# Optimization experiments

Measured on AMD Instinct MI355X. Metric: run time of the kernel, lower is better.

Reference implementation:

```python
import jax, jax.numpy as jnp
import numpy as np

N, E = 100000, 3200000
F_NODE, F_EDGE = 2, 7
H, C = 4, 8
HC = H * C
REG, TGT = 500, 1
NUM_LAYERS = 3
ATT_SLOPE = 0.2   # LeakyReLU inside GATv2 attention
ACT_SLOPE = 0.01  # model-level LeakyReLU default
BN_EPS = 1e-5


def gatv2(x, src, dst, e_attr, Wl, bl, Wr, br, We, att, bias):
    n = x.shape[0]
    xl = (x @ Wl + bl).reshape(n, H, C)          # source transform (messages)
    xr = (x @ Wr + br).reshape(n, H, C)          # destination transform
    ee = (e_attr @ We).reshape(-1, H, C)         # edge transform (no bias in PyG)
    m = jax.nn.leaky_relu(xl[src] + xr[dst] + ee, ATT_SLOPE)  # [Ef,H,C]
    logits = jnp.einsum('ehc,hc->eh', m, att)    # [Ef,H]
    mx = jax.ops.segment_max(logits, dst, num_segments=n)
    ex = jnp.exp(logits - mx[dst])
    den = jax.ops.segment_sum(ex, dst, num_segments=n)
    alpha = ex / (den[dst] + 1e-16)              # edge-softmax grouped by dst
    out = jax.ops.segment_sum(xl[src] * alpha[:, :, None], dst, num_segments=n)
    return out.reshape(n, HC) + bias             # concat heads + bias


def setup_inputs() -> dict:
    key = jax.random.key(0)
    ks = jax.random.split(key, 30)
    # edges with no self loops (module calls add_self_loops on top)
    s = jax.random.randint(ks[0], (E,), 0, N, dtype=jnp.int32)
    off = jax.random.randint(ks[1], (E,), 1, N, dtype=jnp.int32)
    d = (s + off) % N
    edge_index = jnp.stack([s, d])
    x = jax.random.normal(ks[2], (N, F_NODE), dtype=jnp.float32)
    edge_attr = jax.random.normal(ks[3], (E, F_EDGE), dtype=jnp.float32)

    def glorot(k, shape):
        fan = shape[0] + shape[-1]
        return jax.random.normal(k, shape, dtype=jnp.float32) * jnp.sqrt(2.0 / fan)

    inp = dict(x=x, edge_index=edge_index, edge_attr=edge_attr)
    i = 4
    for tag, fin in (("1", F_NODE), ("2", HC)):
        inp["Wl" + tag] = glorot(ks[i], (fin, HC)); i += 1
        inp["bl" + tag] = jnp.zeros((HC,), jnp.float32)
        inp["Wr" + tag] = glorot(ks[i], (fin, HC)); i += 1
        inp["br" + tag] = jnp.zeros((HC,), jnp.float32)
        inp["We" + tag] = glorot(ks[i], (F_EDGE, HC)); i += 1
        inp["att" + tag] = glorot(ks[i], (H, C)); i += 1
        inp["b" + tag] = jnp.zeros((HC,), jnp.float32)
    inp["gamma"] = jnp.ones((HC,), jnp.float32)
    inp["beta"] = jnp.zeros((HC,), jnp.float32)
    inp["Wreg"] = glorot(ks[i], (HC, REG)); i += 1
    inp["breg"] = jnp.zeros((REG,), jnp.float32)
    inp["Wend"] = glorot(ks[i], (REG, TGT)); i += 1
    inp["bend"] = jnp.zeros((TGT,), jnp.float32)
    return inp


def reference(x, edge_index, edge_attr,
              Wl1, bl1, Wr1, br1, We1, att1, b1,
              Wl2, bl2, Wr2, br2, We2, att2, b2,
              gamma, beta, Wreg, breg, Wend, bend):
    n = x.shape[0]
    loop = jnp.arange(n, dtype=edge_index.dtype)
    srcf = jnp.concatenate([edge_index[0], loop])
    dstf = jnp.concatenate([edge_index[1], loop])
    # self-loop edge attrs filled with mean (PyG fill_value='mean')
    ea_mean = jnp.mean(edge_attr, axis=0, keepdims=True)
    eaf = jnp.concatenate([edge_attr, jnp.broadcast_to(ea_mean, (n, edge_attr.shape[1]))])

    h = gatv2(x, srcf, dstf, eaf, Wl1, bl1, Wr1, br1, We1, att1, b1)
    for _ in range(NUM_LAYERS - 1):
        mu = jnp.mean(h, axis=0)
        var = jnp.var(h, axis=0)
        h = (h - mu) * jax.lax.rsqrt(var + BN_EPS) * gamma + beta
        h = jax.nn.leaky_relu(h, ACT_SLOPE)
        h = gatv2(h, srcf, dstf, eaf, Wl2, bl2, Wr2, br2, We2, att2, b2)
    h = jax.nn.leaky_relu(h, ACT_SLOPE)
    h = h @ Wreg + breg
    return h @ Wend + bend
```

## Files before the change

### kernel.cpp

```cpp
#include <hip/hip_runtime.h>
#include <hip/hip_fp16.h>
#include <math.h>

#define NN 100000
#define EE 3200000
#define FE 7
#define GNB 32
#define CRR 1024
#define NBK 391
#define BKCAP 8688
#define T1 4096
#define FB1 ((EE + T1 - 1) / T1)

typedef unsigned int uivec4 __attribute__((ext_vector_type(4)));
static __device__ __forceinline__ uint4 ntload4(const uint4* p) {
    uivec4 v = __builtin_nontemporal_load((const uivec4*)p);
    uint4 r; r.x = v.x; r.y = v.y; r.z = v.z; r.w = v.w; return r;
}

static __device__ __forceinline__ __half2 hmax2(__half2 a, __half2 b) {
    unsigned int ua = *(unsigned int*)&a, ub = *(unsigned int*)&b, ur;
    asm("v_pk_max_f16 %0, %1, %2" : "=v"(ur) : "v"(ua), "v"(ub));
    return *(__half2*)&ur;
}


__global__ void k_ea_sum(const float* __restrict__ ea, double* __restrict__ ea_sum) {
    float acc[FE];
#pragma unroll
    for (int f = 0; f < FE; ++f) acc[f] = 0.f;
    int stride = gridDim.x * blockDim.x;
    for (int e = blockIdx.x * blockDim.x + threadIdx.x; e < EE; e += stride) {
        const float* r = ea + (size_t)e * FE;
#pragma unroll
        for (int f = 0; f < FE; ++f) acc[f] += r[f];
    }
    __shared__ float part[4][FE];
    int wave = threadIdx.x >> 6;
#pragma unroll
    for (int f = 0; f < FE; ++f) {
        float v = acc[f];
        for (int o = 32; o > 0; o >>= 1) v += __shfl_down(v, o, 64);
        if ((threadIdx.x & 63) == 0) part[wave][f] = v;
    }
    __syncthreads();
    if (threadIdx.x < FE) {
        float s = part[0][threadIdx.x] + part[1][threadIdx.x] +
                  part[2][threadIdx.x] + part[3][threadIdx.x];
        atomicAdd(&ea_sum[threadIdx.x], (double)s);
    }
}

__global__ void k_ea_mean(const double* __restrict__ ea_sum, float* __restrict__ ea_mean) {
    int f = threadIdx.x;
    if (f < 8) ea_mean[f] = (f < FE) ? (float)(ea_sum[f] / (double)EE) : 0.f;
}

__global__ void k_ginit(int* __restrict__ gbucket) {
    int b = blockIdx.x * blockDim.x + threadIdx.x;
    if (b < NBK) gbucket[b] = b * BKCAP;
}

__global__ __launch_bounds__(512) void k_fill1(const int* __restrict__ ei,
                                               const float* __restrict__ ea,
                                               int* __restrict__ gbucket,
                                               uint4* __restrict__ srt) {
    __shared__ int hbin[NBK];
    for (int i = threadIdx.x; i < NBK; i += 512) hbin[i] = 0;
    __syncthreads();
    int e0 = blockIdx.x * T1;
    int rb[8];
#pragma unroll
    for (int i = 0; i < 8; ++i) {
        int e = e0 + i * 512 + threadIdx.x;
        int v = -1;
        if (e < EE) {
            int d = __builtin_nontemporal_load(ei + EE + e);
            int b = d >> 8;
            int r = atomicAdd(&hbin[b], 1);
            v = (r << 17) | ((d & 255) << 9) | b;
        }
        rb[i] = v;
    }
    __syncthreads();
    for (int i = threadIdx.x; i < NBK; i += 512) {
        int c = hbin[i];
        hbin[i] = (c > 0) ? atomicAdd(&gbucket[i], c) : 0;
    }
    __syncthreads();
#pragma unroll
    for (int i = 0; i < 8; ++i) {
        int v = rb[i];
        if (v < 0) continue;
        int e = e0 + i * 512 + threadIdx.x;
        int b = v & 511;
        unsigned dl = (unsigned)((v >> 9) & 255);
        int r = v >> 17;
        int pos = hbin[b] + r;
        int s = __builtin_nontemporal_load(ei + e);
        const float* rr = ea + (size_t)e * FE;
        unsigned h[FE];
#pragma unroll
        for (int f = 0; f < FE; ++f) {
            float af = __builtin_nontemporal_load(rr + f);
            h[f] = (unsigned)__half_as_ushort(__float2half_rn(af));
        }
#pragma unroll
        for (int f = 0; f < 6; ++f) { h[f] = (h[f] + 1) >> 1; if (h[f] > 0x7FFFu) h[f] = 0x7FFFu; }
        unsigned h6 = (h[6] + 4) >> 3; if (h6 > 0x1FFFu) h6 = 0x1FFFu;
        uint4 u;
        u.x = h[0] | (h[1] << 15) | ((dl & 3u) << 30);
        u.y = h[2] | (h[3] << 15) | (((dl >> 2) & 3u) << 30);
        u.z = h[4] | (h[5] << 15) | (((dl >> 4) & 3u) << 30);
        u.w = (unsigned)s | (h6 << 17) | ((dl >> 6) << 30);
        srt[(size_t)pos] = u;
    }
}

__global__ __launch_bounds__(512) void k_bscan(const int* __restrict__ gbucket,
                                               int* __restrict__ bbase) {
    __shared__ int ts[512];
    int t = threadIdx.x;
    int c = (t < NBK) ? (gbucket[t] - t * BKCAP) : 0;
    ts[t] = c;
    __syncthreads();
    for (int o = 1; o < 512; o <<= 1) {
        int u = (t >= o) ? ts[t - o] : 0;
        __syncthreads();
        ts[t] += u;
        __syncthreads();
    }
    if (t < NBK) bbase[t] = ts[t] - c;
}

__global__ __launch_bounds__(512) void k_fill2(const uint4* __restrict__ srt,
                                               const int* __restrict__ gbucket,
                                               const int* __restrict__ bbase,
                                               int* __restrict__ offs,
                                               uint4* __restrict__ rec) {
    __shared__ int hist[256], hcopy[256], strt[256];
    int t = threadIdx.x;
    int b = blockIdx.x;
    int nbase = b << 8;
    int nb = NN - nbase; if (nb > 256) nb = 256;
    int sbase = b * BKCAP;
    int cnt = gbucket[b] - sbase;
    int bb = bbase[b];
    if (t < 256) hist[t] = 0;
    __syncthreads();
    for (int p = t; p < cnt; p += 512) {
        uint4 s = srt[(size_t)(sbase + p)];
        int dl = (int)((s.x >> 30) | ((s.y >> 30) << 2) | ((s.z >> 30) << 4) | ((s.w >> 30) << 6));
        atomicAdd(&hist[dl], 1);
    }
    __syncthreads();
    if (t < 256) hcopy[t] = hist[t];
    __syncthreads();
    for (int o = 1; o < 256; o <<= 1) {
        int u = 0;
        if (t < 256 && t >= o) u = hist[t - o];
        __syncthreads();
        if (t < 256) hist[t] += u;
        __syncthreads();
    }
    if (t < 256) {
        int c = hcopy[t];
        int start = bb + hist[t] - c;
        strt[t] = start;
        if (t < nb) offs[nbase + t] = start + c;
    }
    __syncthreads();
    for (int p = t; p < cnt; p += 512) {
        uint4 s = srt[(size_t)(sbase + p)];
        int dl = (int)((s.x >> 30) | ((s.y >> 30) << 2) | ((s.z >> 30) << 4) | ((s.w >> 30) << 6));
        int pos = atomicAdd(&strt[dl], 1);
        uint4 u;
        u.x = ((s.x & 0x7FFFu) << 1) | (((s.x >> 15) & 0x7FFFu) << 17);
        u.y = ((s.y & 0x7FFFu) << 1) | (((s.y >> 15) & 0x7FFFu) << 17);
        u.z = ((s.z & 0x7FFFu) << 1) | (((s.z >> 15) & 0x7FFFu) << 17);
        u.w = (s.w & 0x1FFFFu) | (((s.w >> 17) & 0x1FFFu) << 19);
        rec[(size_t)pos] = u;
    }
}

template <int FIN, bool BN>
__global__ void k_xform(const float* __restrict__ h,
                        const float* __restrict__ Wl, const float* __restrict__ bl,
                        const float* __restrict__ Wr, const float* __restrict__ br,
                        const double* __restrict__ bn_sum, const double* __restrict__ bn_sumsq,
                        const float* __restrict__ gamma, const float* __restrict__ beta,
                        __half* __restrict__ xl, __half* __restrict__ xr) {
    __shared__ float sWl[FIN * 32], sWr[FIN * 32], sb[64];
    __shared__ float smu[FIN], ssc[FIN], sbe[FIN];
    for (int i = threadIdx.x; i < FIN * 32; i += blockDim.x) { sWl[i] = Wl[i]; sWr[i] = Wr[i]; }
    if (threadIdx.x < 32) { sb[threadIdx.x] = bl[threadIdx.x]; sb[32 + threadIdx.x] = br[threadIdx.x]; }
    if (BN && threadIdx.x < FIN) {
        int f = threadIdx.x;
        double mu = bn_sum[f] * (1.0 / NN);
        double var = bn_sumsq[f] * (1.0 / NN) - mu * mu;
        smu[f] = (float)mu;
        ssc[f] = gamma[f] * (float)(1.0 / sqrt(var + 1e-5));
        sbe[f] = beta[f];
    }
    __syncthreads();
    int idx = blockIdx.x * blockDim.x + threadIdx.x;
    if (idx >= NN * 32) return;
    int n = idx >> 5, c = idx & 31;
    const float* hr = h + (size_t)n * FIN;
    float al = sb[c], ar = sb[32 + c];
#pragma unroll
    for (int f = 0; f < FIN; ++f) {
        float v = hr[f];
        if (BN) {
            v = fmaf(v - smu[f], ssc[f], sbe[f]);
            v = v > 0.f ? v : 0.01f * v;
        }
        al = fmaf(v, sWl[f * 32 + c], al);
        ar = fmaf(v, sWr[f * 32 + c], ar);
    }
    xl[idx] = __float2half(al);
    xr[idx] = __float2half(ar);
}

__global__ __launch_bounds__(256) void k_gat_t(
    const int* __restrict__ offs, const uint4* __restrict__ rec,
    const __half* __restrict__ xl, const __half* __restrict__ xr,
    const float* __restrict__ We, const float* __restrict__ att,
    const float* __restrict__ bias, const float* __restrict__ ea_mean,
    float* __restrict__ hout) {
    __shared__ uint4 srec[CRR];
    int n0 = blockIdx.x * GNB;
    int g = threadIdx.x >> 3, j = threadIdx.x & 7, c0 = j * 4;
    int node = n0 + g;

    __half2 weh[FE][2];
#pragma unroll
    for (int f = 0; f < FE; ++f) {
        weh[f][0] = __floats2half2_rn(We[f * 32 + c0], We[f * 32 + c0 + 1]);
        weh[f][1] = __floats2half2_rn(We[f * 32 + c0 + 2], We[f * 32 + c0 + 3]);
    }
    float at0 = att[c0], at1 = att[c0 + 1], at2 = att[c0 + 2], at3 = att[c0 + 3];
    float eam[FE];
#pragma unroll
    for (int f = 0; f < FE; ++f) eam[f] = ea_mean[f];

    float2 rawr = *(const float2*)(xr + (size_t)node * 32 + c0);
    __half2 qh01 = *(const __half2*)&rawr.x;
    __half2 qh23 = *(const __half2*)&rawr.y;
    float2 q01 = __half22float2(qh01);
    float2 q23 = __half22float2(qh23);

    int s_g = (node == 0) ? 0 : offs[node - 1];
    int e_g = offs[node];
    int range0 = (n0 == 0) ? 0 : offs[n0 - 1];
    int range1 = offs[n0 + GNB - 1];

    float sm = 0.f, acc0 = 0.f, acc1 = 0.f, acc2 = 0.f, acc3 = 0.f;
    const __half2 c02 = __float2half2_rn(0.2f);

    auto edge_op = [&](uint4 u, float2 rawl) {
        __half2 lh01 = *(const __half2*)&rawl.x;
        __half2 lh23 = *(const __half2*)&rawl.y;
        __half2 ah01 = *(const __half2*)&u.x;
        __half2 ah23 = *(const __half2*)&u.y;
        __half2 ah45 = *(const __half2*)&u.z;
        __half a6h = __ushort_as_half((unsigned short)((u.w >> 16) & 0xFFFEu));
        __half2 e01 = qh01, e23 = qh23;
        __half2 bc;
        bc = __low2half2(ah01);  e01 = __hfma2(bc, weh[0][0], e01); e23 = __hfma2(bc, weh[0][1], e23);
        bc = __high2half2(ah01); e01 = __hfma2(bc, weh[1][0], e01); e23 = __hfma2(bc, weh[1][1], e23);
        bc = __low2half2(ah23);  e01 = __hfma2(bc, weh[2][0], e01); e23 = __hfma2(bc, weh[2][1], e23);
        bc = __high2half2(ah23); e01 = __hfma2(bc, weh[3][0], e01); e23 = __hfma2(bc, weh[3][1], e23);
        bc = __low2half2(ah45);  e01 = __hfma2(bc, weh[4][0], e01); e23 = __hfma2(bc, weh[4][1], e23);
        bc = __high2half2(ah45); e01 = __hfma2(bc, weh[5][0], e01); e23 = __hfma2(bc, weh[5][1], e23);
        bc = __half2half2(a6h);  e01 = __hfma2(bc, weh[6][0], e01); e23 = __hfma2(bc, weh[6][1], e23);
        __half2 v01 = __hadd2(e01, lh01);
        __half2 v23 = __hadd2(e23, lh23);
        v01 = hmax2(v01, __hmul2(v01, c02));
        v23 = hmax2(v23, __hmul2(v23, c02));
        float2 f01 = __half22float2(v01), f23 = __half22float2(v23);
        float pl = fmaf(f01.x, at0, fmaf(f01.y, at1, fmaf(f23.x, at2, f23.y * at3)));
        float L = pl + __shfl_xor(pl, 1, 64);
        float ex = __expf(L);
        sm += ex;
        float2 l01 = __half22float2(lh01), l23 = __half22float2(lh23);
        acc0 = fmaf(ex, l01.x, acc0);
        acc1 = fmaf(ex, l01.y, acc1);
        acc2 = fmaf(ex, l23.x, acc2);
        acc3 = fmaf(ex, l23.y, acc3);
    };

    for (int base = range0; base < range1; base += CRR) {
        int cnt = range1 - base; if (cnt > CRR) cnt = CRR;
        __syncthreads();
        for (int i = threadIdx.x; i < cnt; i += 256)
            srec[i] = ntload4(&rec[(size_t)base + i]);
        __syncthreads();
        int lo = s_g > base ? s_g : base;
        int hi = e_g < base + cnt ? e_g : base + cnt;
        if (lo >= hi) continue;
        int i1 = lo + 1 < hi ? lo + 1 : hi - 1;
        int i2 = lo + 2 < hi ? lo + 2 : hi - 1;
        uint4 ua = srec[lo - base];
        float2 ra = *(const float2*)(xl + (size_t)(ua.w & 0x1FFFFu) * 32 + c0);
        uint4 ub = srec[i1 - base];
        float2 rb = *(const float2*)(xl + (size_t)(ub.w & 0x1FFFFu) * 32 + c0);
        uint4 uc = srec[i2 - base];
        float2 rc = *(const float2*)(xl + (size_t)(uc.w & 0x1FFFFu) * 32 + c0);
#pragma unroll 3
        for (int p = lo; p < hi; ++p) {
            uint4 cu = ua; float2 cr = ra;
            ua = ub; ra = rb;
            ub = uc; rb = rc;
            int pn = p + 3 < hi ? p + 3 : hi - 1;
            uc = srec[pn - base];
            rc = *(const float2*)(xl + (size_t)(uc.w & 0x1FFFFu) * 32 + c0);
            edge_op(cu, cr);
        }
    }

    {
        float2 rawl = *(const float2*)(xl + (size_t)node * 32 + c0);
        float2 l01 = __half22float2(*(const __half2*)&rawl.x);
        float2 l23 = __half22float2(*(const __half2*)&rawl.y);
        float ee0 = q01.x, ee1 = q01.y, ee2 = q23.x, ee3 = q23.y;
        float wef[FE][4];
#pragma unroll
        for (int f = 0; f < FE; ++f) {
            float2 w0 = __half22float2(weh[f][0]);
            float2 w1 = __half22float2(weh[f][1]);
            wef[f][0] = w0.x; wef[f][1] = w0.y; wef[f][2] = w1.x; wef[f][3] = w1.y;
        }
#pragma unroll
        for (int f = 0; f < FE; ++f) {
            ee0 = fmaf(eam[f], wef[f][0], ee0);
            ee1 = fmaf(eam[f], wef[f][1], ee1);
            ee2 = fmaf(eam[f], wef[f][2], ee2);
            ee3 = fmaf(eam[f], wef[f][3], ee3);
        }
        float v0 = ee0 + l01.x;
        float v1 = ee1 + l01.y;
        float v2 = ee2 + l23.x;
        float v3 = ee3 + l23.y;
        v0 = fmaxf(v0, 0.2f * v0);
        v1 = fmaxf(v1, 0.2f * v1);
        v2 = fmaxf(v2, 0.2f * v2);
        v3 = fmaxf(v3, 0.2f * v3);
        float pl = fmaf(v0, at0, fmaf(v1, at1, fmaf(v2, at2, v3 * at3)));
        float L = pl + __shfl_xor(pl, 1, 64);
        float ex = __expf(L);
        sm += ex;
        acc0 = fmaf(ex, l01.x, acc0);
        acc1 = fmaf(ex, l01.y, acc1);
        acc2 = fmaf(ex, l23.x, acc2);
        acc3 = fmaf(ex, l23.y, acc3);
    }

    float inv = 1.f / (sm + 1e-16f);
    float4 o;
    o.x = fmaf(acc0, inv, bias[c0 + 0]);
    o.y = fmaf(acc1, inv, bias[c0 + 1]);
    o.z = fmaf(acc2, inv, bias[c0 + 2]);
    o.w = fmaf(acc3, inv, bias[c0 + 3]);
    *(float4*)(hout + (size_t)node * 32 + c0) = o;
}

__global__ void k_bn_stats(const float* __restrict__ h, double* __restrict__ bn_sum,
                           double* __restrict__ bn_sumsq) {
    int c = threadIdx.x & 31;
    int row0 = (blockIdx.x * blockDim.x + threadIdx.x) >> 5;
    int rstride = (gridDim.x * blockDim.x) >> 5;
    float s = 0.f, s2 = 0.f;
    for (int n = row0; n < NN; n += rstride) {
        float v = h[(size_t)n * 32 + c];
        s += v;
        s2 = fmaf(v, v, s2);
    }
    s += __shfl_down(s, 32, 64);
    s2 += __shfl_down(s2, 32, 64);
    __shared__ float ls[4][32], ls2[4][32];
    int w = threadIdx.x >> 6;
    if ((threadIdx.x & 63) < 32) { ls[w][c] = s; ls2[w][c] = s2; }
    __syncthreads();
    if (threadIdx.x < 32) {
        float tsum = 0.f, tsq = 0.f;
        for (int i = 0; i < 4; ++i) { tsum += ls[i][threadIdx.x]; tsq += ls2[i][threadIdx.x]; }
        atomicAdd(&bn_sum[threadIdx.x], (double)tsum);
        atomicAdd(&bn_sumsq[threadIdx.x], (double)tsq);
    }
}

__global__ void k_wend(const float* __restrict__ Wreg, const float* __restrict__ breg,
                       const float* __restrict__ Wend, const float* __restrict__ bend,
                       float* __restrict__ wend, float* __restrict__ c0v) {
    int t = threadIdx.x;
    if (t < 32) {
        float s = 0.f;
        for (int k = 0; k < 500; ++k) s = fmaf(Wreg[t * 500 + k], Wend[k], s);
        wend[t] = s;
    } else if (t == 32) {
        float s = 0.f;
        for (int k = 0; k < 500; ++k) s = fmaf(breg[k], Wend[k], s);
        *c0v = s + bend[0];
    }
}

__global__ void k_out(const float* __restrict__ h, const float* __restrict__ wend,
                      const float* __restrict__ c0v, float* __restrict__ out) {
    int n = blockIdx.x * blockDim.x + threadIdx.x;
    if (n >= NN) return;
    const float* r = h + (size_t)n * 32;
    float s = *c0v;
#pragma unroll
    for (int c = 0; c < 32; ++c) {
        float v = r[c];
        v = v > 0.f ? v : 0.01f * v;
        s = fmaf(v, wend[c], s);
    }
    out[n] = s;
}

extern "C" void kernel_launch(void* const* d_in, const int* in_sizes, int n_in,
                              void* d_out, int out_size, void* d_ws, size_t ws_size,
                              hipStream_t stream) {
    (void)in_sizes; (void)n_in; (void)out_size; (void)ws_size;
    const float* x    = (const float*)d_in[0];
    const int*   ei   = (const int*)d_in[1];
    const float* ea   = (const float*)d_in[2];
    const float* Wl1  = (const float*)d_in[3];
    const float* bl1  = (const float*)d_in[4];
    const float* Wr1  = (const float*)d_in[5];
    const float* br1  = (const float*)d_in[6];
    const float* We1  = (const float*)d_in[7];
    const float* att1 = (const float*)d_in[8];
    const float* b1   = (const float*)d_in[9];
    const float* Wl2  = (const float*)d_in[10];
    const float* bl2  = (const float*)d_in[11];
    const float* Wr2  = (const float*)d_in[12];
    const float* br2  = (const float*)d_in[13];
    const float* We2  = (const float*)d_in[14];
    const float* att2 = (const float*)d_in[15];
    const float* b2   = (const float*)d_in[16];
    const float* gamma= (const float*)d_in[17];
    const float* beta = (const float*)d_in[18];
    const float* Wreg = (const float*)d_in[19];
    const float* breg = (const float*)d_in[20];
    const float* Wend = (const float*)d_in[21];
    const float* bend = (const float*)d_in[22];
    float* out = (float*)d_out;

    char* w = (char*)d_ws;
    double* ea_sum   = (double*)(w + 0);
    double* bn_sum   = (double*)(w + 64);
    double* bn_sumsq = (double*)(w + 320);
    float*  ea_mean  = (float*)(w + 576);
    float*  wend     = (float*)(w + 608);
    float*  c0v      = (float*)(w + 736);
    int*    gbucket  = (int*)(w + 2048);
    int*    bbase    = (int*)(w + 4096);
    size_t o = 8192;
    int* offs = (int*)(w + o); o += ((size_t)NN * 4 + 255) & ~(size_t)255;
    __half* xl = (__half*)(w + o); o += ((size_t)NN * 32 * 2 + 255) & ~(size_t)255;
    __half* xr = (__half*)(w + o); o += ((size_t)NN * 32 * 2 + 255) & ~(size_t)255;
    float* hb = (float*)(w + o); o += (size_t)NN * 32 * 4;
    uint4* rec = (uint4*)(w + o); o += (size_t)EE * 16;
    uint4* srt = (uint4*)(w + o); o += (size_t)NBK * BKCAP * 16;

    hipMemsetAsync(w, 0, 1024, stream);

    k_ea_sum<<<2048, 256, 0, stream>>>(ea, ea_sum);
    k_ea_mean<<<1, 64, 0, stream>>>(ea_sum, ea_mean);
    k_ginit<<<2, 256, 0, stream>>>(gbucket);
    k_fill1<<<FB1, 512, 0, stream>>>(ei, ea, gbucket, srt);
    k_bscan<<<1, 512, 0, stream>>>(gbucket, bbase);
    k_fill2<<<NBK, 512, 0, stream>>>(srt, gbucket, bbase, offs, rec);
    k_wend<<<1, 64, 0, stream>>>(Wreg, breg, Wend, bend, wend, c0v);

    const int xbl = (NN * 32 + 255) / 256;
    const int gbl = NN / GNB;

    k_xform<2, false><<<xbl, 256, 0, stream>>>(x, Wl1, bl1, Wr1, br1,
                                               bn_sum, bn_sumsq, gamma, beta, xl, xr);
    k_gat_t<<<gbl, 256, 0, stream>>>(offs, rec, xl, xr, We1, att1, b1, ea_mean, hb);

    for (int it = 0; it < 2; ++it) {
        hipMemsetAsync(w + 64, 0, 512, stream);
        k_bn_stats<<<1024, 256, 0, stream>>>(hb, bn_sum, bn_sumsq);
        k_xform<32, true><<<xbl, 256, 0, stream>>>(hb, Wl2, bl2, Wr2, br2,
                                                   bn_sum, bn_sumsq, gamma, beta, xl, xr);
        k_gat_t<<<gbl, 256, 0, stream>>>(offs, rec, xl, xr, We2, att2, b2, ea_mean, hb);
    }

    k_out<<<(NN + 255) / 256, 256, 0, stream>>>(hb, wend, c0v, out);
}
```

Before: 781.3 us.

## Fuse edge-attr mean, BN statistics and output head into neighboring kernels

The edge-attribute column sums now accumulate inside k_fill1, which already streams edge_attr, so the separate full pass over that array goes away. BatchNorm sum and sum-of-squares are gathered in the GAT kernel epilogue with shared-memory atomics, removing the separate k_bn_stats pass over h. The final LeakyReLU plus folded regression head is computed in the last GAT layer, which then skips writing h, replacing k_out. The small setup kernels are merged, and the ea_mean computation moves into k_bscan, so there are fewer launches; the cost is extra shared-memory atomic contention and register pressure in the GAT and fill kernels.

```diff
diff --git a/kernel.cpp b/kernel.cpp
--- a/kernel.cpp
+++ b/kernel.cpp
@@ -25,47 +25,33 @@
 }
 
 
-__global__ void k_ea_sum(const float* __restrict__ ea, double* __restrict__ ea_sum) {
-    float acc[FE];
-#pragma unroll
-    for (int f = 0; f < FE; ++f) acc[f] = 0.f;
-    int stride = gridDim.x * blockDim.x;
-    for (int e = blockIdx.x * blockDim.x + threadIdx.x; e < EE; e += stride) {
-        const float* r = ea + (size_t)e * FE;
-#pragma unroll
-        for (int f = 0; f < FE; ++f) acc[f] += r[f];
-    }
-    __shared__ float part[4][FE];
-    int wave = threadIdx.x >> 6;
-#pragma unroll
-    for (int f = 0; f < FE; ++f) {
-        float v = acc[f];
-        for (int o = 32; o > 0; o >>= 1) v += __shfl_down(v, o, 64);
-        if ((threadIdx.x & 63) == 0) part[wave][f] = v;
-    }
-    __syncthreads();
-    if (threadIdx.x < FE) {
-        float s = part[0][threadIdx.x] + part[1][threadIdx.x] +
-                  part[2][threadIdx.x] + part[3][threadIdx.x];
-        atomicAdd(&ea_sum[threadIdx.x], (double)s);
-    }
-}
-
-__global__ void k_ea_mean(const double* __restrict__ ea_sum, float* __restrict__ ea_mean) {
-    int f = threadIdx.x;
-    if (f < 8) ea_mean[f] = (f < FE) ? (float)(ea_sum[f] / (double)EE) : 0.f;
-}
-
-__global__ void k_ginit(int* __restrict__ gbucket) {
-    int b = blockIdx.x * blockDim.x + threadIdx.x;
-    if (b < NBK) gbucket[b] = b * BKCAP;
+__global__ void k_prep(const float* __restrict__ Wreg, const float* __restrict__ breg,
+                       const float* __restrict__ Wend, const float* __restrict__ bend,
+                       float* __restrict__ wend, float* __restrict__ c0v,
+                       int* __restrict__ gbucket) {
+    if (blockIdx.x == 0) {
+        int t = threadIdx.x;
+        if (t < 32) {
+            float s = 0.f;
+            for (int k = 0; k < 500; ++k) s = fmaf(Wreg[t * 500 + k], Wend[k], s);
+            wend[t] = s;
+        } else if (t == 32) {
+            float s = 0.f;
+            for (int k = 0; k < 500; ++k) s = fmaf(breg[k], Wend[k], s);
+            *c0v = s + bend[0];
+        }
+    } else {
+        for (int i = threadIdx.x; i < NBK; i += 256) gbucket[i] = i * BKCAP;
+    }
 }
 
 __global__ __launch_bounds__(512) void k_fill1(const int* __restrict__ ei,
                                                const float* __restrict__ ea,
                                                int* __restrict__ gbucket,
-                                               uint4* __restrict__ srt) {
+                                               uint4* __restrict__ srt,
+                                               double* __restrict__ ea_sum) {
     __shared__ int hbin[NBK];
+    __shared__ float part[8][FE];
     for (int i = threadIdx.x; i < NBK; i += 512) hbin[i] = 0;
     __syncthreads();
     int e0 = blockIdx.x * T1;
@@ -88,6 +74,9 @@
         hbin[i] = (c > 0) ? atomicAdd(&gbucket[i], c) : 0;
     }
     __syncthreads();
+    float acc[FE];
+#pragma unroll
+    for (int f = 0; f < FE; ++f) acc[f] = 0.f;
 #pragma unroll
     for (int i = 0; i < 8; ++i) {
         int v = rb[i];
@@ -103,6 +92,7 @@
 #pragma unroll
         for (int f = 0; f < FE; ++f) {
             float af = __builtin_nontemporal_load(rr + f);
+            acc[f] += af;
             h[f] = (unsigned)__half_as_ushort(__float2half_rn(af));
         }
 #pragma unroll
@@ -115,12 +105,29 @@
         u.w = (unsigned)s | (h6 << 17) | ((dl >> 6) << 30);
         srt[(size_t)pos] = u;
     }
+    int wave = threadIdx.x >> 6;
+#pragma unroll
+    for (int f = 0; f < FE; ++f) {
+        float v = acc[f];
+        for (int o = 32; o > 0; o >>= 1) v += __shfl_down(v, o, 64);
+        if ((threadIdx.x & 63) == 0) part[wave][f] = v;
+    }
+    __syncthreads();
+    if (threadIdx.x < FE) {
+        float s = 0.f;
+#pragma unroll
+        for (int i = 0; i < 8; ++i) s += part[i][threadIdx.x];
+        atomicAdd(&ea_sum[threadIdx.x], (double)s);
+    }
 }
 
 __global__ __launch_bounds__(512) void k_bscan(const int* __restrict__ gbucket,
-                                               int* __restrict__ bbase) {
+                                               int* __restrict__ bbase,
+                                               const double* __restrict__ ea_sum,
+                                               float* __restrict__ ea_mean) {
     __shared__ int ts[512];
     int t = threadIdx.x;
+    if (t < 8) ea_mean[t] = (t < FE) ? (float)(ea_sum[t] / (double)EE) : 0.f;
     int c = (t < NBK) ? (gbucket[t] - t * BKCAP) : 0;
     ts[t] = c;
     __syncthreads();
@@ -222,16 +229,22 @@
     xr[idx] = __float2half(ar);
 }
 
+template <int MODE>
 __global__ __launch_bounds__(256) void k_gat_t(
     const int* __restrict__ offs, const uint4* __restrict__ rec,
     const __half* __restrict__ xl, const __half* __restrict__ xr,
     const float* __restrict__ We, const float* __restrict__ att,
     const float* __restrict__ bias, const float* __restrict__ ea_mean,
-    float* __restrict__ hout) {
+    float* __restrict__ hout, double* __restrict__ bn_sum,
+    double* __restrict__ bn_sumsq, const float* __restrict__ wend,
+    const float* __restrict__ c0v, float* __restrict__ out) {
     __shared__ uint4 srec[CRR];
+    __shared__ float bnsum[32], bnsq[32];
     int n0 = blockIdx.x * GNB;
     int g = threadIdx.x >> 3, j = threadIdx.x & 7, c0 = j * 4;
     int node = n0 + g;
+    if (MODE == 1 && threadIdx.x < 32) { bnsum[threadIdx.x] = 0.f; bnsq[threadIdx.x] = 0.f; }
+    __syncthreads();
 
     __half2 weh[FE][2];
 #pragma unroll
@@ -357,67 +370,37 @@
     }
 
     float inv = 1.f / (sm + 1e-16f);
-    float4 o;
-    o.x = fmaf(acc0, inv, bias[c0 + 0]);
-    o.y = fmaf(acc1, inv, bias[c0 + 1]);
-    o.z = fmaf(acc2, inv, bias[c0 + 2]);
-    o.w = fmaf(acc3, inv, bias[c0 + 3]);
-    *(float4*)(hout + (size_t)node * 32 + c0) = o;
-}
-
-__global__ void k_bn_stats(const float* __restrict__ h, double* __restrict__ bn_sum,
-                           double* __restrict__ bn_sumsq) {
-    int c = threadIdx.x & 31;
-    int row0 = (blockIdx.x * blockDim.x + threadIdx.x) >> 5;
-    int rstride = (gridDim.x * blockDim.x) >> 5;
-    float s = 0.f, s2 = 0.f;
-    for (int n = row0; n < NN; n += rstride) {
-        float v = h[(size_t)n * 32 + c];
-        s += v;
-        s2 = fmaf(v, v, s2);
-    }
-    s += __shfl_down(s, 32, 64);
-    s2 += __shfl_down(s2, 32, 64);
-    __shared__ float ls[4][32], ls2[4][32];
-    int w = threadIdx.x >> 6;
-    if ((threadIdx.x & 63) < 32) { ls[w][c] = s; ls2[w][c] = s2; }
-    __syncthreads();
-    if (threadIdx.x < 32) {
-        float tsum = 0.f, tsq = 0.f;
-        for (int i = 0; i < 4; ++i) { tsum += ls[i][threadIdx.x]; tsq += ls2[i][threadIdx.x]; }
-        atomicAdd(&bn_sum[threadIdx.x], (double)tsum);
-        atomicAdd(&bn_sumsq[threadIdx.x], (double)tsq);
-    }
-}
-
-__global__ void k_wend(const float* __restrict__ Wreg, const float* __restrict__ breg,
-                       const float* __restrict__ Wend, const float* __restrict__ bend,
-                       float* __restrict__ wend, float* __restrict__ c0v) {
-    int t = threadIdx.x;
-    if (t < 32) {
-        float s = 0.f;
-        for (int k = 0; k < 500; ++k) s = fmaf(Wreg[t * 500 + k], Wend[k], s);
-        wend[t] = s;
-    } else if (t == 32) {
-        float s = 0.f;
-        for (int k = 0; k < 500; ++k) s = fmaf(breg[k], Wend[k], s);
-        *c0v = s + bend[0];
-    }
-}
-
-__global__ void k_out(const float* __restrict__ h, const float* __restrict__ wend,
-                      const float* __restrict__ c0v, float* __restrict__ out) {
-    int n = blockIdx.x * blockDim.x + threadIdx.x;
-    if (n >= NN) return;
-    const float* r = h + (size_t)n * 32;
-    float s = *c0v;
-#pragma unroll
-    for (int c = 0; c < 32; ++c) {
-        float v = r[c];
-        v = v > 0.f ? v : 0.01f * v;
-        s = fmaf(v, wend[c], s);
-    }
-    out[n] = s;
+    float o0 = fmaf(acc0, inv, bias[c0 + 0]);
+    float o1 = fmaf(acc1, inv, bias[c0 + 1]);
+    float o2 = fmaf(acc2, inv, bias[c0 + 2]);
+    float o3 = fmaf(acc3, inv, bias[c0 + 3]);
+    if (MODE != 2) {
+        float4 o; o.x = o0; o.y = o1; o.z = o2; o.w = o3;
+        *(float4*)(hout + (size_t)node * 32 + c0) = o;
+    }
+    if (MODE == 1) {
+        atomicAdd(&bnsum[c0 + 0], o0); atomicAdd(&bnsq[c0 + 0], o0 * o0);
+        atomicAdd(&bnsum[c0 + 1], o1); atomicAdd(&bnsq[c0 + 1], o1 * o1);
+        atomicAdd(&bnsum[c0 + 2], o2); atomicAdd(&bnsq[c0 + 2], o2 * o2);
+        atomicAdd(&bnsum[c0 + 3], o3); atomicAdd(&bnsq[c0 + 3], o3 * o3);
+        __syncthreads();
+        if (threadIdx.x < 32) {
+            atomicAdd(&bn_sum[threadIdx.x], (double)bnsum[threadIdx.x]);
+            atomicAdd(&bn_sumsq[threadIdx.x], (double)bnsq[threadIdx.x]);
+        }
+    }
+    if (MODE == 2) {
+        float w0 = wend[c0], w1 = wend[c0 + 1], w2 = wend[c0 + 2], w3 = wend[c0 + 3];
+        float p0 = o0 > 0.f ? o0 : 0.01f * o0;
+        float p1 = o1 > 0.f ? o1 : 0.01f * o1;
+        float p2 = o2 > 0.f ? o2 : 0.01f * o2;
+        float p3 = o3 > 0.f ? o3 : 0.01f * o3;
+        float p = fmaf(p0, w0, fmaf(p1, w1, fmaf(p2, w2, p3 * w3)));
+        p += __shfl_xor(p, 1, 64);
+        p += __shfl_xor(p, 2, 64);
+        p += __shfl_xor(p, 4, 64);
+        if (j == 0) out[node] = p + *c0v;
+    }
 }
 
 extern "C" void kernel_launch(void* const* d_in, const int* in_sizes, int n_in,
@@ -468,28 +451,27 @@
 
     hipMemsetAsync(w, 0, 1024, stream);
 
-    k_ea_sum<<<2048, 256, 0, stream>>>(ea, ea_sum);
-    k_ea_mean<<<1, 64, 0, stream>>>(ea_sum, ea_mean);
-    k_ginit<<<2, 256, 0, stream>>>(gbucket);
-    k_fill1<<<FB1, 512, 0, stream>>>(ei, ea, gbucket, srt);
-    k_bscan<<<1, 512, 0, stream>>>(gbucket, bbase);
+    k_prep<<<2, 256, 0, stream>>>(Wreg, breg, Wend, bend, wend, c0v, gbucket);
+    k_fill1<<<FB1, 512, 0, stream>>>(ei, ea, gbucket, srt, ea_sum);
+    k_bscan<<<1, 512, 0, stream>>>(gbucket, bbase, ea_sum, ea_mean);
     k_fill2<<<NBK, 512, 0, stream>>>(srt, gbucket, bbase, offs, rec);
-    k_wend<<<1, 64, 0, stream>>>(Wreg, breg, Wend, bend, wend, c0v);
 
     const int xbl = (NN * 32 + 255) / 256;
     const int gbl = NN / GNB;
 
     k_xform<2, false><<<xbl, 256, 0, stream>>>(x, Wl1, bl1, Wr1, br1,
                                                bn_sum, bn_sumsq, gamma, beta, xl, xr);
-    k_gat_t<<<gbl, 256, 0, stream>>>(offs, rec, xl, xr, We1, att1, b1, ea_mean, hb);
-
-    for (int it = 0; it < 2; ++it) {
-        hipMemsetAsync(w + 64, 0, 512, stream);
-        k_bn_stats<<<1024, 256, 0, stream>>>(hb, bn_sum, bn_sumsq);
-        k_xform<32, true><<<xbl, 256, 0, stream>>>(hb, Wl2, bl2, Wr2, br2,
-                                                   bn_sum, bn_sumsq, gamma, beta, xl, xr);
-        k_gat_t<<<gbl, 256, 0, stream>>>(offs, rec, xl, xr, We2, att2, b2, ea_mean, hb);
-    }
-
-    k_out<<<(NN + 255) / 256, 256, 0, stream>>>(hb, wend, c0v, out);
-}
+    k_gat_t<1><<<gbl, 256, 0, stream>>>(offs, rec, xl, xr, We1, att1, b1, ea_mean,
+                                        hb, bn_sum, bn_sumsq, wend, c0v, out);
+
+    k_xform<32, true><<<xbl, 256, 0, stream>>>(hb, Wl2, bl2, Wr2, br2,
+                                               bn_sum, bn_sumsq, gamma, beta, xl, xr);
+    hipMemsetAsync(w + 64, 0, 512, stream);
+    k_gat_t<1><<<gbl, 256, 0, stream>>>(offs, rec, xl, xr, We2, att2, b2, ea_mean,
+                                        hb, bn_sum, bn_sumsq, wend, c0v, out);
+
+    k_xform<32, true><<<xbl, 256, 0, stream>>>(hb, Wl2, bl2, Wr2, br2,
+                                               bn_sum, bn_sumsq, gamma, beta, xl, xr);
+    k_gat_t<2><<<gbl, 256, 0, stream>>>(offs, rec, xl, xr, We2, att2, b2, ea_mean,
+                                        hb, bn_sum, bn_sumsq, wend, c0v, out);
+}
```

Result: faster. 746.2 us (-4.5%).
